# Optimization experiments

Measured on AMD Instinct MI355X. Metric: run time of the kernel, lower is better.

The kernel has to match this reference:

```python
import jax, jax.numpy as jnp
import numpy as np

N = 50000
E = 1_600_000
IN_DIM = 512
H1, H2 = 2048, 2048
OUT_DIM = 512


def setup_inputs() -> dict:
    key = jax.random.key(0)
    ks = jax.random.split(key, 10)
    x = jax.random.normal(ks[0], (N, IN_DIM), dtype=jnp.float32)
    edge_weight = jax.random.uniform(ks[1], (E,), dtype=jnp.float32)
    edge_src = jax.random.randint(ks[2], (E,), 0, N, dtype=jnp.int32)
    edge_dst = jax.random.randint(ks[3], (E,), 0, N, dtype=jnp.int32)
    s = 0.02  # small init scale for numerical sanity
    W1 = jax.random.normal(ks[4], (2 * IN_DIM, H1), dtype=jnp.float32) * s
    b1 = jnp.zeros((H1,), dtype=jnp.float32)
    W2 = jax.random.normal(ks[5], (H1, H2), dtype=jnp.float32) * s
    b2 = jnp.zeros((H2,), dtype=jnp.float32)
    W3 = jax.random.normal(ks[6], (H2, OUT_DIM), dtype=jnp.float32) * s
    b3 = jnp.zeros((OUT_DIM,), dtype=jnp.float32)
    return {"x": x, "edge_weight": edge_weight, "W1": W1, "b1": b1,
            "W2": W2, "b2": b2, "W3": W3, "b3": b3,
            "edge_src": edge_src, "edge_dst": edge_dst}


def reference(x, edge_weight, W1, b1, W2, b2, W3, b3, edge_src, edge_dst):
    # SpMM: agg[i] = sum_{e: dst=i} w_e * x[src_e]   (A_norm @ x in COO form)
    msgs = edge_weight[:, None] * x[edge_src]          # (E, in_dim)
    agg = jax.ops.segment_sum(msgs, edge_dst, num_segments=N)  # (N, in_dim)
    h = jnp.concatenate([x, agg], axis=1)              # (N, 2*in_dim)
    h = jax.nn.relu(h @ W1 + b1)
    h = jax.nn.relu(h @ W2 + b2)
    return h @ W3 + b3                                 # (N, out_dim)
```

## Files before the change

### kernel.cpp

```cpp
#include <hip/hip_runtime.h>

#define NNODES 50000
#define NEDGES 1600000
#define IN_DIM 512
#define K1 1024
#define H1 2048
#define H2 2048
#define OUT_DIM 512
#define MTILES 196
#define M_PAD 50176
#define SCAN_BLOCKS 49

typedef unsigned short ushort_t;
typedef short sh8 __attribute__((ext_vector_type(8)));
typedef float f32x4 __attribute__((ext_vector_type(4)));

__device__ __forceinline__ ushort_t f2bf(float f) {
    unsigned u = __float_as_uint(f);
    unsigned r = (u + 0x7FFFu + ((u >> 16) & 1u)) >> 16;
    return (ushort_t)r;
}
__device__ __forceinline__ float bf2f(ushort_t h) {
    return __uint_as_float(((unsigned)h) << 16);
}

__global__ void zero_kernel(int* __restrict__ p, int n) {
    int i = blockIdx.x * 256 + threadIdx.x;
    if (i < n) p[i] = 0;
}

__global__ void convert_x_kernel(const float* __restrict__ x, ushort_t* __restrict__ h0) {
    int t = blockIdx.x * 256 + threadIdx.x;
    int n = t >> 7, c = t & 127;
    float4 v = ((const float4*)x)[n * 128 + c];
    ushort4 o;
    o.x = f2bf(v.x); o.y = f2bf(v.y); o.z = f2bf(v.z); o.w = f2bf(v.w);
    ((ushort4*)h0)[n * 256 + c] = o;
}

__global__ void wtrans_kernel(const float* __restrict__ W, ushort_t* __restrict__ Wt,
                              int K, int Nn) {
    __shared__ float t[32][33];
    int n0 = blockIdx.x * 32, k0 = blockIdx.y * 32;
    int tx = threadIdx.x, ty = threadIdx.y;
#pragma unroll
    for (int i = 0; i < 4; i++)
        t[ty + 8 * i][tx] = W[(size_t)(k0 + ty + 8 * i) * Nn + n0 + tx];
    __syncthreads();
#pragma unroll
    for (int i = 0; i < 4; i++)
        Wt[(size_t)(n0 + ty + 8 * i) * K + k0 + tx] = f2bf(t[tx][ty + 8 * i]);
}

__global__ void hist_kernel(const int* __restrict__ edst, int* __restrict__ counts) {
    int e = blockIdx.x * 256 + threadIdx.x;
    atomicAdd(&counts[edst[e]], 1);
}

__global__ void scan_blocks_kernel(const int* __restrict__ counts, int* __restrict__ incl,
                                   int* __restrict__ block_sums) {
    __shared__ int s[1024];
    int b = blockIdx.x, tid = threadIdx.x;
    int i = b * 1024 + tid;
    int c = (i < NNODES) ? counts[i] : 0;
    s[tid] = c;
    __syncthreads();
    for (int off = 1; off < 1024; off <<= 1) {
        int v = (tid >= off) ? s[tid - off] : 0;
        __syncthreads();
        s[tid] += v;
        __syncthreads();
    }
    if (i < NNODES) incl[i] = s[tid];
    if (tid == 1023) block_sums[b] = s[1023];
}

__global__ void scan_sums_kernel(const int* __restrict__ block_sums, int* __restrict__ carry) {
    if (threadIdx.x == 0 && blockIdx.x == 0) {
        int run = 0;
        for (int b = 0; b < SCAN_BLOCKS; b++) { carry[b] = run; run += block_sums[b]; }
    }
}

__global__ void scan_finalize_kernel(const int* __restrict__ counts, const int* __restrict__ incl,
                                     const int* __restrict__ carry, int* __restrict__ offsets,
                                     int* __restrict__ cursor) {
    int b = blockIdx.x, tid = threadIdx.x;
    int i = b * 1024 + tid;
    if (i < NNODES) {
        int v = incl[i] + carry[b];
        offsets[i + 1] = v;
        cursor[i] = v - counts[i];
    }
    if (i == 0) offsets[0] = 0;
}

__global__ void scatter_kernel(const int* __restrict__ edst, int* __restrict__ cursor,
                               int* __restrict__ perm) {
    int e = blockIdx.x * 256 + threadIdx.x;
    int d = edst[e];
    int pos = atomicAdd(&cursor[d], 1);
    perm[pos] = e;
}

__global__ void aggregate_kernel(ushort_t* __restrict__ h0,
                                 const float* __restrict__ ew,
                                 const int* __restrict__ esrc,
                                 const int* __restrict__ offsets,
                                 const int* __restrict__ perm) {
    __shared__ int se[128];
    __shared__ float swt[128];
    int n = blockIdx.x;
    int tid = threadIdx.x;
    int beg = offsets[n], end = offsets[n + 1];
    float a0 = 0.f, a1 = 0.f, a2 = 0.f, a3 = 0.f;
    for (int base = beg; base < end; base += 128) {
        int cnt = end - base; if (cnt > 128) cnt = 128;
        if (tid < cnt) {
            int e = perm[base + tid];
            se[tid] = esrc[e];
            swt[tid] = ew[e];
        }
        __syncthreads();
        for (int j = 0; j < cnt; j++) {
            int s = se[j];
            float w = swt[j];
            ushort4 v = *(const ushort4*)&h0[(size_t)s * 1024 + tid * 4];
            a0 += w * bf2f(v.x);
            a1 += w * bf2f(v.y);
            a2 += w * bf2f(v.z);
            a3 += w * bf2f(v.w);
        }
        __syncthreads();
    }
    ushort4 o;
    o.x = f2bf(a0); o.y = f2bf(a1); o.z = f2bf(a2); o.w = f2bf(a3);
    *(ushort4*)&h0[(size_t)n * 1024 + 512 + tid * 4] = o;
}

#define BAR() do { __builtin_amdgcn_sched_barrier(0); __builtin_amdgcn_s_barrier(); \
                   __builtin_amdgcn_sched_barrier(0); } while (0)

#define STAGE(MAT, HALF, T, D) do {                                                      \
    _Pragma("unroll")                                                                    \
    for (int j = 0; j < 2; j++) {                                                        \
        const ushort_t* src = ((MAT) ? pb[j] : pa[j]) + (size_t)(HALF) * 128 * K + (size_t)(T) * 64; \
        __builtin_amdgcn_global_load_lds(                                                \
            (const __attribute__((address_space(1))) void*)src,                          \
            (__attribute__((address_space(3))) void*)(lds + ((MAT) * 32768u + (D) * 16384u + (HALF) * 8192u + (unsigned)(wid * 2 + j) * 512u)), \
            16, 0, 0);                                                                   \
    }                                                                                    \
} while (0)

#define LDA(DST, MH, RB) do {                                                            \
    _Pragma("unroll")                                                                    \
    for (int mq = 0; mq < 4; mq++)                                                       \
        _Pragma("unroll")                                                                \
        for (int ks = 0; ks < 2; ks++)                                                   \
            DST[mq * 2 + ks] = *(const sh8*)(aL + (RB) + ((MH) * 4 + mq) * 2048 + ks * 1024); \
} while (0)

#define LDB(DST, NH, RB) do {                                                            \
    _Pragma("unroll")                                                                    \
    for (int nq = 0; nq < 2; nq++)                                                       \
        _Pragma("unroll")                                                                \
        for (int ks = 0; ks < 2; ks++)                                                   \
            DST[nq * 2 + ks] = *(const sh8*)(bL + (RB) + ((NH) * 2 + nq) * 2048 + ks * 1024); \
} while (0)

#define MM(AF, BF, MH, NH) do {                                                          \
    __builtin_amdgcn_s_setprio(1);                                                       \
    _Pragma("unroll")                                                                    \
    for (int mq = 0; mq < 4; mq++)                                                       \
        _Pragma("unroll")                                                                \
        for (int nq = 0; nq < 2; nq++)                                                   \
            _Pragma("unroll")                                                            \
            for (int ks = 0; ks < 2; ks++)                                               \
                acc[(MH) * 4 + mq][(NH) * 2 + nq] = __builtin_amdgcn_mfma_f32_16x16x32_bf16( \
                    AF[mq * 2 + ks], BF[nq * 2 + ks], acc[(MH) * 4 + mq][(NH) * 2 + nq], 0, 0, 0); \
    __builtin_amdgcn_s_setprio(0);                                                       \
} while (0)

#define TILE(T, D) do {                                                                  \
    LDA(af0, 0, (D) * 32768); LDB(bf0, 0, (D) * 32768);                                  \
    if ((T) + 1 < NT) STAGE(0, 0, (T) + 1, (D) ^ 1);                                     \
    BAR(); MM(af0, bf0, 0, 0); BAR();                                                    \
    LDB(bf1, 1, (D) * 32768);                                                            \
    if ((T) + 1 < NT) STAGE(0, 1, (T) + 1, (D) ^ 1);                                     \
    BAR(); MM(af0, bf1, 0, 1); BAR();                                                    \
    LDA(af1, 1, (D) * 32768);                                                            \
    if ((T) + 2 < NT) STAGE(1, 0, (T) + 2, (D));                                         \
    BAR(); MM(af1, bf1, 1, 1); BAR();                                                    \
    if ((T) + 2 < NT) {                                                                  \
        STAGE(1, 1, (T) + 2, (D));                                                       \
        asm volatile("s_waitcnt vmcnt(4)" ::: "memory");                                 \
    } else {                                                                             \
        asm volatile("s_waitcnt vmcnt(0)" ::: "memory");                                 \
    }                                                                                    \
    BAR(); MM(af1, bf0, 1, 0); BAR();                                                    \
} while (0)

template <int K, int NOUT, bool RELU, bool OUTBF16>
__launch_bounds__(512, 2)
__global__ void gemm256(const ushort_t* __restrict__ A, const ushort_t* __restrict__ B,
                        const float* __restrict__ bias, void* __restrict__ C, int Mvalid) {
    __shared__ __align__(16) ushort_t lds[65536];
    const int tid = threadIdx.x;
    const int wid = tid >> 6, lane = tid & 63;
    const int lrow = lane & 15, lq = lane >> 4;
    const int wm = wid >> 2, wn = wid & 3;
    const int m0 = blockIdx.y * 256, n0 = blockIdx.x * 256;
    const int NT = K / 64;

    const ushort_t* pa[2];
    const ushort_t* pb[2];
#pragma unroll
    for (int j = 0; j < 2; j++) {
        int p = (wid * 2 + j) * 1024 + lane * 16;
        int q = p ^ (((p >> 9) & 1) << 5);
        int row = ((q >> 11) << 4) | ((q >> 6) & 15);
        int k   = (((q >> 10) & 1) << 5) | ((q & 63) >> 1);
        pa[j] = A + (size_t)(m0 + row) * K + k;
        pb[j] = B + (size_t)(n0 + row) * K + k;
    }

    const int abase = (lrow * 64 + lq * 16) ^ ((lrow & 8) << 2);
    const char* aL = (const char*)lds + wm * 16384 + abase;
    const char* bL = (const char*)lds + 65536 + (wn >> 1) * 16384 + (wn & 1) * 8192 + abase;

    f32x4 acc[8][4] = {};
    sh8 af0[8], af1[8], bf0[4], bf1[4];

    STAGE(0, 0, 0, 0); STAGE(0, 1, 0, 0); STAGE(1, 0, 0, 0); STAGE(1, 1, 0, 0);
    STAGE(1, 0, 1, 1); STAGE(1, 1, 1, 1);
    asm volatile("s_waitcnt vmcnt(4)" ::: "memory");
    BAR();

#pragma unroll 1
    for (int t = 0; t < NT; t += 2) {
        TILE(t, 0);
        TILE(t + 1, 1);
    }

    int gcol[4]; float bv[4];
#pragma unroll
    for (int nn = 0; nn < 4; nn++) {
        gcol[nn] = n0 + wn * 64 + nn * 16 + lrow;
        bv[nn] = bias[gcol[nn]];
    }
#pragma unroll
    for (int mm = 0; mm < 8; mm++) {
#pragma unroll
        for (int r = 0; r < 4; r++) {
            int gm = m0 + wm * 128 + mm * 16 + lq * 4 + r;
#pragma unroll
            for (int nn = 0; nn < 4; nn++) {
                float v = acc[mm][nn][r] + bv[nn];
                if (RELU) v = v > 0.f ? v : 0.f;
                if (OUTBF16) {
                    ((ushort_t*)C)[(size_t)gm * NOUT + gcol[nn]] = f2bf(v);
                } else {
                    if (gm < Mvalid) ((float*)C)[(size_t)gm * NOUT + gcol[nn]] = v;
                }
            }
        }
    }
}

static inline size_t align256(size_t x) { return (x + 255) & ~(size_t)255; }

extern "C" void kernel_launch(void* const* d_in, const int* in_sizes, int n_in,
                              void* d_out, int out_size, void* d_ws, size_t ws_size,
                              hipStream_t stream) {
    const float* x   = (const float*)d_in[0];
    const float* ew  = (const float*)d_in[1];
    const float* W1  = (const float*)d_in[2];
    const float* b1  = (const float*)d_in[3];
    const float* W2  = (const float*)d_in[4];
    const float* b2  = (const float*)d_in[5];
    const float* W3  = (const float*)d_in[6];
    const float* b3  = (const float*)d_in[7];
    const int* esrc  = (const int*)d_in[8];
    const int* edst  = (const int*)d_in[9];
    float* out = (float*)d_out;

    char* ws = (char*)d_ws;
    size_t off = 0;
    ushort_t* h0  = (ushort_t*)(ws + off); off = align256(off + (size_t)M_PAD * 1024 * 2);
    ushort_t* w1t = (ushort_t*)(ws + off); off = align256(off + (size_t)H1 * K1 * 2);
    ushort_t* w2t = (ushort_t*)(ws + off); off = align256(off + (size_t)H2 * H1 * 2);
    ushort_t* w3t = (ushort_t*)(ws + off); off = align256(off + (size_t)OUT_DIM * H2 * 2);
    size_t fixed_end = off;

    const size_t per_tile = (size_t)256 * 2048 * 2 * 2;
    size_t avail = (ws_size > fixed_end + 512) ? (ws_size - fixed_end - 512) : 0;
    int T = (int)(avail / per_tile);
    if (T > MTILES) T = MTILES;
    if (T < 4) T = 4;
    int nchunks = (MTILES + T - 1) / T;
    T = (MTILES + nchunks - 1) / nchunks;

    ushort_t* h1c = (ushort_t*)(ws + fixed_end);
    ushort_t* h2c = (ushort_t*)(ws + fixed_end + (size_t)T * 256 * 2048 * 2);

    size_t coff = fixed_end;
    int* counts     = (int*)(ws + coff); coff = align256(coff + (size_t)NNODES * 4);
    int* offsets    = (int*)(ws + coff); coff = align256(coff + (size_t)(NNODES + 1) * 4);
    int* cursor     = (int*)(ws + coff); coff = align256(coff + (size_t)NNODES * 4);
    int* incl       = (int*)(ws + coff); coff = align256(coff + (size_t)NNODES * 4);
    int* perm       = (int*)(ws + coff); coff = align256(coff + (size_t)NEDGES * 4);
    int* block_sums = (int*)(ws + coff); coff = align256(coff + (size_t)SCAN_BLOCKS * 4);
    int* carry      = (int*)(ws + coff); coff = align256(coff + (size_t)SCAN_BLOCKS * 4);

    zero_kernel<<<(NNODES + 255) / 256, 256, 0, stream>>>(counts, NNODES);

    convert_x_kernel<<<25000, 256, 0, stream>>>(x, h0);

    zero_kernel<<<(90112 + 255) / 256, 256, 0, stream>>>((int*)(h0 + (size_t)NNODES * 1024), 90112);

    wtrans_kernel<<<dim3(H1 / 32, K1 / 32), dim3(32, 8), 0, stream>>>(W1, w1t, K1, H1);
    wtrans_kernel<<<dim3(H2 / 32, H1 / 32), dim3(32, 8), 0, stream>>>(W2, w2t, H1, H2);
    wtrans_kernel<<<dim3(OUT_DIM / 32, H2 / 32), dim3(32, 8), 0, stream>>>(W3, w3t, H2, OUT_DIM);

    hist_kernel<<<NEDGES / 256, 256, 0, stream>>>(edst, counts);
    scan_blocks_kernel<<<SCAN_BLOCKS, 1024, 0, stream>>>(counts, incl, block_sums);
    scan_sums_kernel<<<1, 64, 0, stream>>>(block_sums, carry);
    scan_finalize_kernel<<<SCAN_BLOCKS, 1024, 0, stream>>>(counts, incl, carry, offsets, cursor);
    scatter_kernel<<<NEDGES / 256, 256, 0, stream>>>(edst, cursor, perm);

    aggregate_kernel<<<NNODES, 128, 0, stream>>>(h0, ew, esrc, offsets, perm);

    for (int t0 = 0; t0 < MTILES; t0 += T) {
        int tiles = MTILES - t0; if (tiles > T) tiles = T;
        int row0 = t0 * 256;
        gemm256<K1, H1, true, true><<<dim3(H1 / 256, tiles), 512, 0, stream>>>(
            h0 + (size_t)row0 * K1, w1t, b1, h1c, 0);
        gemm256<H1, H2, true, true><<<dim3(H2 / 256, tiles), 512, 0, stream>>>(
            h1c, w2t, b2, h2c, 0);
        gemm256<H2, OUT_DIM, false, false><<<dim3(OUT_DIM / 256, tiles), 512, 0, stream>>>(
            h2c, w3t, b3, out + (size_t)row0 * OUT_DIM, NNODES - row0);
    }
}
```

Baseline: 1.510 ms.

## Split-K the final GEMM with atomics and batch aggregation gathers

The last GEMM (N=512 output) now splits K=2048 into four slices along grid z. Each slice accumulates into a pre-zeroed fp32 output with atomicAdd, and only slice 0 adds the bias. This is meant to fill more CUs, since that GEMM previously launched only 2 column blocks per row tile. The aggregation kernel also issues eight neighbor gathers before accumulating, to raise memory-level parallelism. The cost is an extra zeroing pass over the output, atomic write traffic, and non-deterministic summation order.

```diff
diff --git a/kernel.cpp b/kernel.cpp
--- a/kernel.cpp
+++ b/kernel.cpp
@@ -122,7 +122,24 @@
             swt[tid] = ew[e];
         }
         __syncthreads();
-        for (int j = 0; j < cnt; j++) {
+        int j = 0;
+        for (; j + 8 <= cnt; j += 8) {
+            ushort4 v[8]; float w[8];
+#pragma unroll
+            for (int u = 0; u < 8; u++) {
+                int s = se[j + u];
+                w[u] = swt[j + u];
+                v[u] = *(const ushort4*)&h0[(size_t)s * 1024 + tid * 4];
+            }
+#pragma unroll
+            for (int u = 0; u < 8; u++) {
+                a0 += w[u] * bf2f(v[u].x);
+                a1 += w[u] * bf2f(v[u].y);
+                a2 += w[u] * bf2f(v[u].z);
+                a3 += w[u] * bf2f(v[u].w);
+            }
+        }
+        for (; j < cnt; j++) {
             int s = se[j];
             float w = swt[j];
             ushort4 v = *(const ushort4*)&h0[(size_t)s * 1024 + tid * 4];
@@ -144,7 +161,7 @@
 #define STAGE(MAT, HALF, T, D) do {                                                      \
     _Pragma("unroll")                                                                    \
     for (int j = 0; j < 2; j++) {                                                        \
-        const ushort_t* src = ((MAT) ? pb[j] : pa[j]) + (size_t)(HALF) * 128 * K + (size_t)(T) * 64; \
+        const ushort_t* src = ((MAT) ? pb[j] : pa[j]) + (size_t)(HALF) * 128 * LDK + (size_t)(T) * 64; \
         __builtin_amdgcn_global_load_lds(                                                \
             (const __attribute__((address_space(1))) void*)src,                          \
             (__attribute__((address_space(3))) void*)(lds + ((MAT) * 32768u + (D) * 16384u + (HALF) * 8192u + (unsigned)(wid * 2 + j) * 512u)), \
@@ -200,7 +217,7 @@
     BAR(); MM(af1, bf0, 1, 0); BAR();                                                    \
 } while (0)
 
-template <int K, int NOUT, bool RELU, bool OUTBF16>
+template <int LDK, int KLEN, int NOUT, bool RELU, int OUTMODE>
 __launch_bounds__(512, 2)
 __global__ void gemm256(const ushort_t* __restrict__ A, const ushort_t* __restrict__ B,
                         const float* __restrict__ bias, void* __restrict__ C, int Mvalid) {
@@ -210,7 +227,8 @@
     const int lrow = lane & 15, lq = lane >> 4;
     const int wm = wid >> 2, wn = wid & 3;
     const int m0 = blockIdx.y * 256, n0 = blockIdx.x * 256;
-    const int NT = K / 64;
+    const int NT = KLEN / 64;
+    const int koff = (OUTMODE == 2) ? blockIdx.z * KLEN : 0;
 
     const ushort_t* pa[2];
     const ushort_t* pb[2];
@@ -220,8 +238,8 @@
         int q = p ^ (((p >> 9) & 1) << 5);
         int row = ((q >> 11) << 4) | ((q >> 6) & 15);
         int k   = (((q >> 10) & 1) << 5) | ((q & 63) >> 1);
-        pa[j] = A + (size_t)(m0 + row) * K + k;
-        pb[j] = B + (size_t)(n0 + row) * K + k;
+        pa[j] = A + (size_t)(m0 + row) * LDK + k + koff;
+        pb[j] = B + (size_t)(n0 + row) * LDK + k + koff;
     }
 
     const int abase = (lrow * 64 + lq * 16) ^ ((lrow & 8) << 2);
@@ -246,7 +264,7 @@
 #pragma unroll
     for (int nn = 0; nn < 4; nn++) {
         gcol[nn] = n0 + wn * 64 + nn * 16 + lrow;
-        bv[nn] = bias[gcol[nn]];
+        bv[nn] = (OUTMODE != 2 || blockIdx.z == 0) ? bias[gcol[nn]] : 0.f;
     }
 #pragma unroll
     for (int mm = 0; mm < 8; mm++) {
@@ -257,10 +275,12 @@
             for (int nn = 0; nn < 4; nn++) {
                 float v = acc[mm][nn][r] + bv[nn];
                 if (RELU) v = v > 0.f ? v : 0.f;
-                if (OUTBF16) {
+                if (OUTMODE == 1) {
                     ((ushort_t*)C)[(size_t)gm * NOUT + gcol[nn]] = f2bf(v);
+                } else if (OUTMODE == 0) {
+                    if (gm < Mvalid) ((float*)C)[(size_t)gm * NOUT + gcol[nn]] = v;
                 } else {
-                    if (gm < Mvalid) ((float*)C)[(size_t)gm * NOUT + gcol[nn]] = v;
+                    if (gm < Mvalid) atomicAdd(&((float*)C)[(size_t)gm * NOUT + gcol[nn]], v);
                 }
             }
         }
@@ -313,6 +333,7 @@
     int* carry      = (int*)(ws + coff); coff = align256(coff + (size_t)SCAN_BLOCKS * 4);
 
     zero_kernel<<<(NNODES + 255) / 256, 256, 0, stream>>>(counts, NNODES);
+    zero_kernel<<<(NNODES * OUT_DIM + 255) / 256, 256, 0, stream>>>((int*)out, NNODES * OUT_DIM);
 
     convert_x_kernel<<<25000, 256, 0, stream>>>(x, h0);
 
@@ -333,11 +354,11 @@
     for (int t0 = 0; t0 < MTILES; t0 += T) {
         int tiles = MTILES - t0; if (tiles > T) tiles = T;
         int row0 = t0 * 256;
-        gemm256<K1, H1, true, true><<<dim3(H1 / 256, tiles), 512, 0, stream>>>(
+        gemm256<K1, K1, H1, true, 1><<<dim3(H1 / 256, tiles), 512, 0, stream>>>(
             h0 + (size_t)row0 * K1, w1t, b1, h1c, 0);
-        gemm256<H1, H2, true, true><<<dim3(H2 / 256, tiles), 512, 0, stream>>>(
+        gemm256<H1, H1, H2, true, 1><<<dim3(H2 / 256, tiles), 512, 0, stream>>>(
             h1c, w2t, b2, h2c, 0);
-        gemm256<H2, OUT_DIM, false, false><<<dim3(OUT_DIM / 256, tiles), 512, 0, stream>>>(
+        gemm256<H2, 512, OUT_DIM, false, 2><<<dim3(OUT_DIM / 256, tiles, 4), 512, 0, stream>>>(
             h2c, w3t, b3, out + (size_t)row0 * OUT_DIM, NNODES - row0);
     }
 }
```

New measurement: 1.822 ms. +20.6%, slower.

## Batch gather loads in aggregation and use smaller-tile GEMM for final layer

Applied to the files above, without the earlier changes.

The aggregation loop now issues eight independent row gathers before accumulating, so more memory requests are in flight per thread. The final layer (N=512) switches from the 256x256-tile GEMM to a new 128x128-tile kernel with 256 threads, which launches four times as many blocks for the narrow output and improves CU occupancy. The new GEMM uses a single-buffered global_load_lds path and may have less latency hiding per block.

```diff
diff --git a/kernel.cpp b/kernel.cpp
--- a/kernel.cpp
+++ b/kernel.cpp
@@ -122,7 +122,24 @@
             swt[tid] = ew[e];
         }
         __syncthreads();
-        for (int j = 0; j < cnt; j++) {
+        int j = 0;
+        for (; j + 8 <= cnt; j += 8) {
+            ushort4 v[8]; float w[8];
+#pragma unroll
+            for (int u = 0; u < 8; u++) {
+                int s = se[j + u];
+                w[u] = swt[j + u];
+                v[u] = *(const ushort4*)&h0[(size_t)s * 1024 + tid * 4];
+            }
+#pragma unroll
+            for (int u = 0; u < 8; u++) {
+                a0 += w[u] * bf2f(v[u].x);
+                a1 += w[u] * bf2f(v[u].y);
+                a2 += w[u] * bf2f(v[u].z);
+                a3 += w[u] * bf2f(v[u].w);
+            }
+        }
+        for (; j < cnt; j++) {
             int s = se[j];
             float w = swt[j];
             ushort4 v = *(const ushort4*)&h0[(size_t)s * 1024 + tid * 4];
@@ -267,6 +284,75 @@
     }
 }
 
+template <int K, int NOUT, bool RELU, bool OUTBF16>
+__launch_bounds__(256)
+__global__ void gemm_bt(const ushort_t* __restrict__ A, const ushort_t* __restrict__ B,
+                        const float* __restrict__ bias, void* __restrict__ C, int Mvalid) {
+    __shared__ __align__(16) ushort_t As[128 * 32];
+    __shared__ __align__(16) ushort_t Bs[128 * 32];
+    int tid = threadIdx.x;
+    int wid = tid >> 6, lane = tid & 63;
+    int m0 = blockIdx.y * 128, n0 = blockIdx.x * 128;
+    int wm = (wid >> 1) * 64, wn = (wid & 1) * 64;
+    int lrow = lane & 15, lq = lane >> 4;
+
+    f32x4 acc[4][4] = {};
+
+#pragma unroll 1
+    for (int k0 = 0; k0 < K; k0 += 32) {
+#pragma unroll
+        for (int j = 0; j < 2; j++) {
+            int cb = wid * 128 + j * 64;
+            int ch = cb + lane;
+            int row = ch >> 2, kc = ch & 3;
+            const ushort_t* ga = A + (size_t)(m0 + row) * K + k0 + kc * 8;
+            __builtin_amdgcn_global_load_lds(
+                (const __attribute__((address_space(1))) void*)ga,
+                (__attribute__((address_space(3))) void*)(As + (size_t)cb * 8), 16, 0, 0);
+            const ushort_t* gb = B + (size_t)(n0 + row) * K + k0 + kc * 8;
+            __builtin_amdgcn_global_load_lds(
+                (const __attribute__((address_space(1))) void*)gb,
+                (__attribute__((address_space(3))) void*)(Bs + (size_t)cb * 8), 16, 0, 0);
+        }
+        __syncthreads();
+
+        sh8 af[4], bfr[4];
+#pragma unroll
+        for (int mm = 0; mm < 4; mm++)
+            af[mm] = *(const sh8*)&As[(wm + mm * 16 + lrow) * 32 + lq * 8];
+#pragma unroll
+        for (int nn = 0; nn < 4; nn++)
+            bfr[nn] = *(const sh8*)&Bs[(wn + nn * 16 + lrow) * 32 + lq * 8];
+#pragma unroll
+        for (int mm = 0; mm < 4; mm++)
+#pragma unroll
+            for (int nn = 0; nn < 4; nn++)
+                acc[mm][nn] = __builtin_amdgcn_mfma_f32_16x16x32_bf16(
+                    af[mm], bfr[nn], acc[mm][nn], 0, 0, 0);
+        __syncthreads();
+    }
+
+#pragma unroll
+    for (int nn = 0; nn < 4; nn++) {
+        int gn = n0 + wn + nn * 16 + lrow;
+        float bv = bias[gn];
+#pragma unroll
+        for (int mm = 0; mm < 4; mm++) {
+#pragma unroll
+            for (int r = 0; r < 4; r++) {
+                int gm = m0 + wm + mm * 16 + lq * 4 + r;
+                float v = acc[mm][nn][r] + bv;
+                if (RELU) v = v > 0.f ? v : 0.f;
+                if (OUTBF16) {
+                    ((ushort_t*)C)[(size_t)gm * NOUT + gn] = f2bf(v);
+                } else {
+                    if (gm < Mvalid) ((float*)C)[(size_t)gm * NOUT + gn] = v;
+                }
+            }
+        }
+    }
+}
+
 static inline size_t align256(size_t x) { return (x + 255) & ~(size_t)255; }
 
 extern "C" void kernel_launch(void* const* d_in, const int* in_sizes, int n_in,
@@ -337,7 +423,7 @@
             h0 + (size_t)row0 * K1, w1t, b1, h1c, 0);
         gemm256<H1, H2, true, true><<<dim3(H2 / 256, tiles), 512, 0, stream>>>(
             h1c, w2t, b2, h2c, 0);
-        gemm256<H2, OUT_DIM, false, false><<<dim3(OUT_DIM / 256, tiles), 512, 0, stream>>>(
+        gemm_bt<H2, OUT_DIM, false, false><<<dim3(OUT_DIM / 128, tiles * 2), 256, 0, stream>>>(
             h2c, w3t, b3, out + (size_t)row0 * OUT_DIM, NNODES - row0);
     }
 }
```

New measurement: 1.648 ms. 9.1% more time.
